# Kernel optimization log

Hardware: AMD Instinct MI355X
Metric: run time of the kernel (lower is better)

The kernel has to match this reference:

```python
import jax, jax.numpy as jnp
import numpy as np

NEG_SLOPE = 0.01  # torch LeakyReLU default
VAR = 0.1


def _leaky(z):
    return jnp.where(z >= 0, z, NEG_SLOPE * z)


def _sconv(theta, bias, L, x):
    # theta: (C_out, C_in, 2), L: (M, M), x: (B, C_in, M)
    Lx = jnp.einsum('mn,bin->bim', L, x)                     # degree-1 Laplacian term
    y = jnp.einsum('oi,bim->bom', theta[:, :, 0], x) \
        + jnp.einsum('oi,bim->bom', theta[:, :, 1], Lx)
    if bias is not None:
        y = y + bias
    return y


def setup_inputs() -> dict:
    key = jax.random.key(0)
    ks = iter(jax.random.split(key, 32))
    B, Cin = 8, 4
    Ms = [2000, 6000, 4000]
    inp = {}
    for d, M in enumerate(Ms):
        inp[f'L{d}'] = jax.random.normal(next(ks), (M, M), jnp.float32) / np.sqrt(M)
        inp[f'x{d}'] = jax.random.normal(next(ks), (B, Cin, M), jnp.float32)
        inp[f'th{d}_1'] = VAR * jax.random.normal(next(ks), (16, 4, 2), jnp.float32)
        inp[f'b{d}_1'] = jnp.zeros((1, 16, 1), jnp.float32)
        inp[f'th{d}_2'] = VAR * jax.random.normal(next(ks), (32, 16, 2), jnp.float32)
    dims = [(96, 64), (64, 32), (32, 16), (16, 2)]
    for i, (din, dout) in enumerate(dims, start=1):
        bound = 1.0 / np.sqrt(din)
        inp[f'W{i}'] = jax.random.uniform(next(ks), (dout, din), jnp.float32, -bound, bound)
        inp[f'bb{i}'] = jax.random.uniform(next(ks), (dout,), jnp.float32, -bound, bound)
    return inp


def reference(L0, L1, L2, x0, x1, x2,
              th0_1, b0_1, th0_2,
              th1_1, b1_1, th1_2,
              th2_1, b2_1, th2_2,
              W1, bb1, W2, bb2, W3, bb3, W4, bb4):
    out0_1 = _sconv(th0_1, b0_1, L0, x0)
    out1_1 = _sconv(th1_1, b1_1, L1, x1)
    out2_1 = _sconv(th2_1, b2_1, L2, x2)
    out0_2 = _sconv(th0_2, None, L0, _leaky(out0_1))   # (B, 32, M0)
    out1_2 = _sconv(th1_2, None, L1, _leaky(out1_1))
    out2_2 = _sconv(th2_2, None, L2, _leaky(out2_1))
    # mean-pool over simplices, concat along channel dim -> (B, 96)
    pooled = jnp.concatenate([out0_2.mean(axis=2), out1_2.mean(axis=2), out2_2.mean(axis=2)], axis=1)
    h = pooled @ W1.T + bb1      # dropouts are identity at inference
    h = h @ W2.T + bb2
    h = h @ W3.T + bb3
    logits = h @ W4.T + bb4      # (B, 2)
    return (logits, out0_2, out1_2, out2_2)
```

## Files before the change

### kernel.cpp

```cpp
#include <hip/hip_runtime.h>
#include <stdint.h>

typedef __attribute__((ext_vector_type(4))) float f32x4;
typedef __attribute__((ext_vector_type(8))) __bf16 bf16x8;

constexpr int MS_[3] = {2000, 6000, 4000};
constexpr int MP_[3] = {2048, 6144, 4096};
constexpr int RB_[3] = {32, 96, 64};
constexpr int NTILE = 192;
constexpr long long OUT_OFF_[3] = {16, 512016, 2048016};

constexpr int S1_[3] = {8, 16, 16};
constexpr int KS1_[3] = {256, 384, 256};
constexpr int NG1 = 1536 + 1024 + 256;
constexpr int KS2_[3] = {512, 1536, 1024};
constexpr int NG2 = 768 + 512 + 256;

__device__ __forceinline__ unsigned short f2bf(float f) {
  __bf16 b = (__bf16)f;
  return *reinterpret_cast<unsigned short*>(&b);
}

__device__ __forceinline__ void gload_lds16(const void* g, void* l) {
  __builtin_amdgcn_global_load_lds(
      (const __attribute__((address_space(1))) unsigned int*)g,
      (__attribute__((address_space(3))) unsigned int*)l, 16, 0, 0);
}

__device__ __forceinline__ void bar_pin() {
  __builtin_amdgcn_s_barrier();
  __builtin_amdgcn_sched_barrier(0);
}

__device__ __forceinline__ void tile_decode(int bid, int& d, int& t) {
  if (bid < RB_[0]) { d = 0; t = bid; }
  else if (bid < RB_[0] + RB_[1]) { d = 1; t = bid - RB_[0]; }
  else { d = 2; t = bid - RB_[0] - RB_[1]; }
}

struct PrepArgs {
  const float* x[3];
  unsigned short* xT[3];
  float* zero0; int zero_n;
};

__global__ __launch_bounds__(256) void prep_k(PrepArgs pa) {
  int d, t; tile_decode(blockIdx.x, d, t);
  const int M = MS_[d], Mp = MP_[d];
  const float* x = pa.x[d];
  unsigned short* xT = pa.xT[d];
  const int tid = threadIdx.x;
  const int m0 = t * 64;
  const int ml = tid & 63, cg = tid >> 6;
  const int m = m0 + ml;
  const bool valid = m < M;
#pragma unroll
  for (int it = 0; it < 8; ++it) {
    int c = it * 4 + cg;
    float v = valid ? x[(size_t)c * M + m] : 0.f;
    xT[(size_t)c * Mp + m] = f2bf(v);
  }
  if (blockIdx.x == 0) {
    for (int i = tid; i < pa.zero_n; i += 256) pa.zero0[i] = 0.f;
  }
}

struct GArgs {
  const float* L[3];
  const unsigned short* B[3];
  float* P[3];
};

template <int PASS>
__global__ __launch_bounds__(256, 2) void gemm_k(GArgs ga) {
  int bid = blockIdx.x;
  int d, r, s, nh = 0;
  if constexpr (PASS == 1) {
    if (bid < 1536) { d = 1; r = bid % 96; s = bid / 96; }
    else if (bid < 2560) { bid -= 1536; d = 2; r = bid % 64; s = bid / 64; }
    else { bid -= 2560; d = 0; r = bid % 32; s = bid / 32; }
  } else {
    if (bid < 768) { d = 1; r = bid % 96; int q = bid / 96; nh = q & 1; s = q >> 1; }
    else if (bid < 1280) { bid -= 768; d = 2; r = bid % 64; int q = bid / 64; nh = q & 1; s = q >> 1; }
    else { bid -= 1280; d = 0; r = bid % 32; int q = bid / 32; nh = q & 1; s = q >> 1; }
  }
  const int M = MS_[d], Mp = MP_[d];
  const int KS = (PASS == 1) ? KS1_[d] : KS2_[d];
  const int ns = KS >> 6;
  constexpr int BN = (PASS == 1) ? 32 : 64;
  constexpr int PW = (PASS == 1) ? 32 : 128;
  constexpr int RING = (PASS == 1) ? 4 : 3;
  constexpr int NR = BN / 16;
  constexpr int BI = BN / 32;

  const float* __restrict__ Lp = ga.L[d];
  const unsigned short* __restrict__ Bt = ga.B[d];
  float* __restrict__ Pp = ga.P[d];

  const int m0 = r * 64;
  const int kt0 = s * KS;

  __shared__ __align__(16) char Al[RING][64 * 256];
  __shared__ __align__(16) char Bl[RING][BN * 128];

  const int tid = threadIdx.x;
  const int lane = tid & 63;
  const int wave = tid >> 6;
  const int lr = lane & 15, lk = lane >> 4;

  const float* pAsrc[4];
  int koffA[4];
#pragma unroll
  for (int j = 0; j < 4; ++j) {
    int ldsb = j * 4096 + tid * 16;
    int row = ldsb >> 8;
    int inner = (ldsb & 255) ^ ((row & 7) << 5);
    int grow = m0 + row;
    if (grow > M - 1) grow = M - 1;
    pAsrc[j] = Lp + (size_t)grow * M;
    koffA[j] = inner >> 2;
  }
  const unsigned short* srcB[BI];
#pragma unroll
  for (int j = 0; j < BI; ++j) {
    int ldsb = j * 4096 + tid * 16;
    int col = ldsb >> 7;
    int inner = (ldsb & 127) ^ ((col & 7) << 4);
    srcB[j] = Bt + (size_t)(nh * 64 + col) * Mp + (inner >> 1);
  }

  f32x4 acc[NR];
#pragma unroll
  for (int n = 0; n < NR; ++n) acc[n] = (f32x4){0.f, 0.f, 0.f, 0.f};

  auto mstep = [&](int x) { return x < ns ? x : ns - 1; };
  auto stage = [&](int slot, int step) {
    const int kt = kt0 + step * 64;
#pragma unroll
    for (int j = 0; j < 4; ++j) {
      int gk = kt + koffA[j];
      if (gk + 4 > M) gk = 0;
      gload_lds16(pAsrc[j] + gk, &Al[slot][j * 4096 + tid * 16]);
    }
#pragma unroll
    for (int j = 0; j < BI; ++j)
      gload_lds16(srcB[j] + kt, &Bl[slot][j * 4096 + tid * 16]);
  };
  auto compute = [&](int slot) {
    const char* Ab = &Al[slot][0];
    const char* Bb = &Bl[slot][0];
    const int rowl = wave * 16 + lr;
    const int abase = rowl * 256;
    const int aswz = (rowl & 7) << 5;
    bf16x8 af[2];
#pragma unroll
    for (int kk = 0; kk < 2; ++kk) {
      int off = abase + ((kk * 128 + lk * 32) ^ aswz);
      f32x4 v0 = *reinterpret_cast<const f32x4*>(Ab + off);
      f32x4 v1 = *reinterpret_cast<const f32x4*>(Ab + off + 16);
#pragma unroll
      for (int j = 0; j < 4; ++j) {
        af[kk][j] = (__bf16)v0[j];
        af[kk][4 + j] = (__bf16)v1[j];
      }
    }
#pragma unroll
    for (int nr = 0; nr < NR; ++nr) {
      const int col = nr * 16 + lr;
      const int bbase = col * 128, bswz = (col & 7) << 4;
      bf16x8 b0 = *reinterpret_cast<const bf16x8*>(Bb + bbase + ((lk * 16) ^ bswz));
      bf16x8 b1 = *reinterpret_cast<const bf16x8*>(Bb + bbase + ((64 + lk * 16) ^ bswz));
      acc[nr] = __builtin_amdgcn_mfma_f32_16x16x32_bf16(af[0], b0, acc[nr], 0, 0, 0);
      acc[nr] = __builtin_amdgcn_mfma_f32_16x16x32_bf16(af[1], b1, acc[nr], 0, 0, 0);
    }
  };

  stage(0, 0);
  stage(1, mstep(1));
  if constexpr (RING == 4) stage(2, mstep(2));

  for (int t = 0; t < ns; ++t) {
    if constexpr (PASS == 1) asm volatile("s_waitcnt vmcnt(10)" ::: "memory");
    else                     asm volatile("s_waitcnt vmcnt(6)" ::: "memory");
    bar_pin();
    stage((t + RING - 1) % RING, mstep(t + RING - 1));
    compute(t % RING);
  }

  const int rowb = m0 + wave * 16 + lk * 4;
#pragma unroll
  for (int nr = 0; nr < NR; ++nr) {
    const int cc = (PASS == 1 ? 0 : nh * 64) + nr * 16 + lr;
#pragma unroll
    for (int j = 0; j < 4; ++j)
      Pp[((size_t)s * Mp + rowb + j) * PW + cc] = acc[nr][j];
  }
}

struct EpiAArgs {
  const float* part1[3];
  const float* x[3];
  const float* th1[3];
  const float* b1[3];
  unsigned short* zT[3];
};

__global__ __launch_bounds__(256) void epiA_k(EpiAArgs ea) {
  int d, t; tile_decode(blockIdx.x, d, t);
  const int M = MS_[d], Mp = MP_[d];
  const int m0 = t * 64;
  __shared__ float Ys[32 * 66];
  __shared__ float Xs[32 * 66];
  const int tid = threadIdx.x;
  const float* part = ea.part1[d];
  const size_t st = (size_t)Mp * 32;
  const int S1 = S1_[d];
#pragma unroll
  for (int it = 0; it < 8; ++it) {
    int idx = it * 256 + tid;
    int m = idx >> 5, c = idx & 31;
    size_t base = (size_t)(m0 + m) * 32 + c;
    float ssum = 0.f;
    for (int s5 = 0; s5 < S1; ++s5) ssum += part[s5 * st + base];
    Ys[c * 66 + m] = ssum;
  }
  {
    const float* x = ea.x[d];
    int m = tid & 63, cg = tid >> 6;
    bool valid = (m0 + m) < M;
#pragma unroll
    for (int it = 0; it < 8; ++it) {
      int c = it * 4 + cg;
      Xs[c * 66 + m] = valid ? x[(size_t)c * M + m0 + m] : 0.f;
    }
  }
  __syncthreads();
  const float* th = ea.th1[d];
  const float* bias = ea.b1[d];
  unsigned short* zT = ea.zT[d];
  const int m = tid & 63, cog = tid >> 6;
  const bool valid = (m0 + m) < M;
#pragma unroll
  for (int it = 0; it < 32; ++it) {
    int co = it * 4 + cog;
    int o = co & 15, b = co >> 4;
    float a = bias[o];
#pragma unroll
    for (int i = 0; i < 4; ++i) {
      int ci = b * 4 + i;
      a += th[(o * 4 + i) * 2] * Xs[ci * 66 + m] + th[(o * 4 + i) * 2 + 1] * Ys[ci * 66 + m];
    }
    float zz = (a >= 0.f) ? a : 0.01f * a;
    zT[(size_t)co * Mp + m0 + m] = valid ? f2bf(zz) : (unsigned short)0;
  }
}

struct EpiBArgs {
  const float* part2[3];
  const unsigned short* zT[3];
  const float* th2[3];
  float* out;
  float* csz;
  float* csy;
};

__global__ __launch_bounds__(256) void epiB_k(EpiBArgs eb) {
  int d, t; tile_decode(blockIdx.x, d, t);
  const int M = MS_[d], Mp = MP_[d];
  const int m0 = t * 64;
  __shared__ float Ys[128 * 66];
  __shared__ float red[256];
  const int tid = threadIdx.x;
  const float* part = eb.part2[d];
  float csum = 0.f;
#pragma unroll
  for (int it = 0; it < 32; ++it) {
    int idx = it * 256 + tid;
    int m = idx >> 7, c = idx & 127;
    size_t base = (size_t)(m0 + m) * 128 + c;
    size_t st = (size_t)Mp * 128;
    float ssum = part[base] + part[st + base] + part[2 * st + base] + part[3 * st + base];
    Ys[c * 66 + m] = ssum;
    if (m0 + m < M) csum += ssum;
  }
  red[tid] = csum;
  __syncthreads();
  if (tid < 128) atomicAdd(&eb.csy[d * 128 + tid], red[tid] + red[tid + 128]);

  const unsigned short* zT = eb.zT[d];
  const float* th = eb.th2[d];
  float* outp = eb.out + OUT_OFF_[d];
  const int m = tid & 63, g = tid >> 6;
  const bool valid = (m0 + m) < M;
#pragma unroll
  for (int bb = 0; bb < 2; ++bb) {
    int b = g * 2 + bb;
    float zv[16], yv[16];
#pragma unroll
    for (int o1 = 0; o1 < 16; ++o1) {
      int c = b * 16 + o1;
      unsigned short raw = zT[(size_t)c * Mp + m0 + m];
      __bf16 bf = *reinterpret_cast<__bf16*>(&raw);
      zv[o1] = (float)bf;
      yv[o1] = Ys[c * 66 + m];
    }
#pragma unroll
    for (int o1 = 0; o1 < 16; ++o1) {
      float v = zv[o1];
#pragma unroll
      for (int off = 32; off > 0; off >>= 1) v += __shfl_xor(v, off, 64);
      if (m == 0) atomicAdd(&eb.csz[d * 128 + b * 16 + o1], v);
    }
#pragma unroll
    for (int o2 = 0; o2 < 32; ++o2) {
      float v = 0.f;
#pragma unroll
      for (int o1 = 0; o1 < 16; ++o1)
        v += th[(o2 * 16 + o1) * 2] * zv[o1] + th[(o2 * 16 + o1) * 2 + 1] * yv[o1];
      if (valid) outp[(size_t)(b * 32 + o2) * M + m0 + m] = v;
    }
  }
}

struct MlpArgs {
  const float* csz; const float* csy;
  const float* th2[3];
  const float* W1; const float* b1;
  const float* W2; const float* b2;
  const float* W3; const float* b3;
  const float* W4; const float* b4;
  float* out;
};

__global__ __launch_bounds__(256) void mlp_k(MlpArgs ma) {
  __shared__ float pl[8][96];
  __shared__ float h1[8][64];
  __shared__ float h2[8][32];
  __shared__ float h3[8][16];
  const int tid = threadIdx.x;
  for (int id = tid; id < 768; id += 256) {
    int d = id >> 8, rem = id & 255, b = rem >> 5, o2 = rem & 31;
    const float* th = ma.th2[d];
    float invM = 1.f / (float)MS_[d];
    float v = 0.f;
    for (int o1 = 0; o1 < 16; ++o1)
      v += th[(o2 * 16 + o1) * 2] * ma.csz[d * 128 + b * 16 + o1] +
           th[(o2 * 16 + o1) * 2 + 1] * ma.csy[d * 128 + b * 16 + o1];
    pl[b][d * 32 + o2] = v * invM;
  }
  __syncthreads();
  for (int id = tid; id < 512; id += 256) {
    int b = id >> 6, j = id & 63;
    float v = ma.b1[j];
    for (int k = 0; k < 96; ++k) v += pl[b][k] * ma.W1[j * 96 + k];
    h1[b][j] = v;
  }
  __syncthreads();
  {
    int b = tid >> 5, j = tid & 31;
    float v = ma.b2[j];
    for (int k = 0; k < 64; ++k) v += h1[b][k] * ma.W2[j * 64 + k];
    h2[b][j] = v;
  }
  __syncthreads();
  if (tid < 128) {
    int b = tid >> 4, j = tid & 15;
    float v = ma.b3[j];
    for (int k = 0; k < 32; ++k) v += h2[b][k] * ma.W3[j * 32 + k];
    h3[b][j] = v;
  }
  __syncthreads();
  if (tid < 16) {
    int b = tid >> 1, j = tid & 1;
    float v = ma.b4[j];
    for (int k = 0; k < 16; ++k) v += h3[b][k] * ma.W4[j * 16 + k];
    ma.out[tid] = v;
  }
}

extern "C" void kernel_launch(void* const* d_in, const int* in_sizes, int n_in,
                              void* d_out, int out_size, void* d_ws, size_t ws_size,
                              hipStream_t stream) {
  (void)in_sizes; (void)n_in; (void)out_size; (void)ws_size;
  const float* L[3]   = {(const float*)d_in[0], (const float*)d_in[5], (const float*)d_in[10]};
  const float* x[3]   = {(const float*)d_in[1], (const float*)d_in[6], (const float*)d_in[11]};
  const float* th1[3] = {(const float*)d_in[2], (const float*)d_in[7], (const float*)d_in[12]};
  const float* b1[3]  = {(const float*)d_in[3], (const float*)d_in[8], (const float*)d_in[13]};
  const float* th2[3] = {(const float*)d_in[4], (const float*)d_in[9], (const float*)d_in[14]};
  const float* W1 = (const float*)d_in[15]; const float* bb1 = (const float*)d_in[16];
  const float* W2 = (const float*)d_in[17]; const float* bb2 = (const float*)d_in[18];
  const float* W3 = (const float*)d_in[19]; const float* bb3 = (const float*)d_in[20];
  const float* W4 = (const float*)d_in[21]; const float* bb4 = (const float*)d_in[22];
  float* out = (float*)d_out;

  char* ws = (char*)d_ws;
  size_t off = 0;
  auto alloc = [&](size_t bytes) {
    size_t r = off;
    off = (off + bytes + 255) & ~(size_t)255;
    return r;
  };
  const int MPs[3] = {2048, 6144, 4096};
  unsigned short* xT[3]; unsigned short* zT[3]; float* pb[3];
  for (int d = 0; d < 3; ++d) xT[d] = (unsigned short*)(ws + alloc((size_t)32 * MPs[d] * 2));
  for (int d = 0; d < 3; ++d) zT[d] = (unsigned short*)(ws + alloc((size_t)128 * MPs[d] * 2));
  for (int d = 0; d < 3; ++d) pb[d] = (float*)(ws + alloc((size_t)16 * MPs[d] * 32 * 4));
  float* csz = (float*)(ws + alloc((size_t)3 * 128 * 4));
  float* csy = (float*)(ws + alloc((size_t)3 * 128 * 4));

  PrepArgs pa;
  for (int d = 0; d < 3; ++d) { pa.x[d] = x[d]; pa.xT[d] = xT[d]; }
  pa.zero0 = csz; pa.zero_n = 768;
  prep_k<<<NTILE, 256, 0, stream>>>(pa);

  GArgs g1;
  for (int d = 0; d < 3; ++d) { g1.L[d] = L[d]; g1.B[d] = xT[d]; g1.P[d] = pb[d]; }
  gemm_k<1><<<NG1, 256, 0, stream>>>(g1);

  EpiAArgs ea;
  for (int d = 0; d < 3; ++d) {
    ea.part1[d] = pb[d]; ea.x[d] = x[d]; ea.th1[d] = th1[d]; ea.b1[d] = b1[d]; ea.zT[d] = zT[d];
  }
  epiA_k<<<NTILE, 256, 0, stream>>>(ea);

  GArgs g2;
  for (int d = 0; d < 3; ++d) { g2.L[d] = L[d]; g2.B[d] = zT[d]; g2.P[d] = pb[d]; }
  gemm_k<2><<<NG2, 256, 0, stream>>>(g2);

  EpiBArgs eb;
  for (int d = 0; d < 3; ++d) { eb.part2[d] = pb[d]; eb.zT[d] = zT[d]; eb.th2[d] = th2[d]; }
  eb.out = out; eb.csz = csz; eb.csy = csy;
  epiB_k<<<NTILE, 256, 0, stream>>>(eb);

  MlpArgs ma;
  ma.csz = csz; ma.csy = csy;
  for (int d = 0; d < 3; ++d) ma.th2[d] = th2[d];
  ma.W1 = W1; ma.b1 = bb1; ma.W2 = W2; ma.b2 = bb2;
  ma.W3 = W3; ma.b3 = bb3; ma.W4 = W4; ma.b4 = bb4;
  ma.out = out;
  mlp_k<<<1, 256, 0, stream>>>(ma);
}
```

Measured before the change: 226.1 us.

## Pre-convert Laplacians to bf16 once and widen pass-2 GEMM tile to 128 columns

Adds a conversion kernel that writes each fp32 Laplacian to a bf16 copy in workspace. Both GEMM passes then stream the bf16 copy, halving A-operand traffic and dropping the per-step fp32-to-bf16 conversion in the inner loop. Pass 2 now covers all 128 columns in one block instead of splitting into two 64-column halves, so L is read once per pass rather than twice. The cost is an extra full read of L in fp32 plus a bf16 write before pass 1; ring depths, wait counts and occupancy are retuned, and the old path is kept as a fallback when the workspace is too small.

```diff
diff --git a/kernel.cpp b/kernel.cpp
--- a/kernel.cpp
+++ b/kernel.cpp
@@ -14,7 +14,8 @@
 constexpr int KS1_[3] = {256, 384, 256};
 constexpr int NG1 = 1536 + 1024 + 256;
 constexpr int KS2_[3] = {512, 1536, 1024};
-constexpr int NG2 = 768 + 512 + 256;
+constexpr int NG2 = 384 + 256 + 128;
+constexpr int NCONV = 2304 + 1024 + 256;
 
 __device__ __forceinline__ unsigned short f2bf(float f) {
   __bf16 b = (__bf16)f;
@@ -32,10 +33,42 @@
   __builtin_amdgcn_sched_barrier(0);
 }
 
+template <int W>
+__device__ __forceinline__ void wait_w() {
+  if constexpr (W == 0) asm volatile("s_waitcnt vmcnt(0)" ::: "memory");
+  else if constexpr (W == 5) asm volatile("s_waitcnt vmcnt(5)" ::: "memory");
+  else if constexpr (W == 6) asm volatile("s_waitcnt vmcnt(6)" ::: "memory");
+}
+
 __device__ __forceinline__ void tile_decode(int bid, int& d, int& t) {
   if (bid < RB_[0]) { d = 0; t = bid; }
   else if (bid < RB_[0] + RB_[1]) { d = 1; t = bid - RB_[0]; }
   else { d = 2; t = bid - RB_[0] - RB_[1]; }
+}
+
+struct ConvArgs {
+  const float* src[3];
+  unsigned short* dst[3];
+};
+
+__global__ __launch_bounds__(256) void conv_k(ConvArgs ca) {
+  int bid = blockIdx.x;
+  int d, lb, nb;
+  if (bid < 2304) { d = 1; lb = bid; nb = 2304; }
+  else if (bid < 3328) { d = 2; lb = bid - 2304; nb = 1024; }
+  else { d = 0; lb = bid - 3328; nb = 256; }
+  const float* __restrict__ s = ca.src[d];
+  unsigned short* __restrict__ o = ca.dst[d];
+  const long long n8 = (long long)MS_[d] * MS_[d] / 8;
+  for (long long i = (long long)lb * 256 + threadIdx.x; i < n8; i += (long long)nb * 256) {
+    const float* p = s + i * 8;
+    f32x4 v0 = *reinterpret_cast<const f32x4*>(p);
+    f32x4 v1 = *reinterpret_cast<const f32x4*>(p + 4);
+    union { unsigned short u[8]; int4 q; } pk;
+#pragma unroll
+    for (int j = 0; j < 4; ++j) { pk.u[j] = f2bf(v0[j]); pk.u[4 + j] = f2bf(v1[j]); }
+    *reinterpret_cast<int4*>(o + i * 8) = pk.q;
+  }
 }
 
 struct PrepArgs {
@@ -67,40 +100,43 @@
 
 struct GArgs {
   const float* L[3];
+  const unsigned short* Lb[3];
   const unsigned short* B[3];
   float* P[3];
 };
 
-template <int PASS>
-__global__ __launch_bounds__(256, 2) void gemm_k(GArgs ga) {
+template <int PASS, bool ABF>
+__global__ __launch_bounds__(256, (PASS == 1 && ABF) ? 3 : 2) void gemm_k(GArgs ga) {
   int bid = blockIdx.x;
-  int d, r, s, nh = 0;
+  int d, r, s;
   if constexpr (PASS == 1) {
     if (bid < 1536) { d = 1; r = bid % 96; s = bid / 96; }
     else if (bid < 2560) { bid -= 1536; d = 2; r = bid % 64; s = bid / 64; }
     else { bid -= 2560; d = 0; r = bid % 32; s = bid / 32; }
   } else {
-    if (bid < 768) { d = 1; r = bid % 96; int q = bid / 96; nh = q & 1; s = q >> 1; }
-    else if (bid < 1280) { bid -= 768; d = 2; r = bid % 64; int q = bid / 64; nh = q & 1; s = q >> 1; }
-    else { bid -= 1280; d = 0; r = bid % 32; int q = bid / 32; nh = q & 1; s = q >> 1; }
+    if (bid < 384) { d = 1; r = bid % 96; s = bid / 96; }
+    else if (bid < 640) { bid -= 384; d = 2; r = bid % 64; s = bid / 64; }
+    else { bid -= 640; d = 0; r = bid % 32; s = bid / 32; }
   }
   const int M = MS_[d], Mp = MP_[d];
   const int KS = (PASS == 1) ? KS1_[d] : KS2_[d];
   const int ns = KS >> 6;
-  constexpr int BN = (PASS == 1) ? 32 : 64;
-  constexpr int PW = (PASS == 1) ? 32 : 128;
-  constexpr int RING = (PASS == 1) ? 4 : 3;
+  constexpr int BN = (PASS == 1) ? 32 : 128;
+  constexpr int PW = BN;
   constexpr int NR = BN / 16;
-  constexpr int BI = BN / 32;
-
-  const float* __restrict__ Lp = ga.L[d];
+  constexpr int BIB = BN / 32;
+  constexpr int BIA = ABF ? 2 : 4;
+  constexpr int RING = (PASS == 1) ? (ABF ? 4 : 3) : (ABF ? 3 : 2);
+  constexpr int ABYT = ABF ? 8192 : 16384;
+  constexpr int W = (PASS == 1) ? (ABF ? 6 : 5) : (ABF ? 6 : 0);
+
   const unsigned short* __restrict__ Bt = ga.B[d];
   float* __restrict__ Pp = ga.P[d];
 
   const int m0 = r * 64;
   const int kt0 = s * KS;
 
-  __shared__ __align__(16) char Al[RING][64 * 256];
+  __shared__ __align__(16) char Al[RING][ABYT];
   __shared__ __align__(16) char Bl[RING][BN * 128];
 
   const int tid = threadIdx.x;
@@ -108,25 +144,34 @@
   const int wave = tid >> 6;
   const int lr = lane & 15, lk = lane >> 4;
 
-  const float* pAsrc[4];
-  int koffA[4];
-#pragma unroll
-  for (int j = 0; j < 4; ++j) {
+  const char* rowA[BIA];
+  int koffA[BIA];
+#pragma unroll
+  for (int j = 0; j < BIA; ++j) {
     int ldsb = j * 4096 + tid * 16;
-    int row = ldsb >> 8;
-    int inner = (ldsb & 255) ^ ((row & 7) << 5);
+    int row, koff;
+    if constexpr (ABF) {
+      row = ldsb >> 7;
+      int inner = (ldsb & 127) ^ ((row & 7) << 4);
+      koff = inner >> 1;
+    } else {
+      row = ldsb >> 8;
+      int inner = (ldsb & 255) ^ ((row & 7) << 5);
+      koff = inner >> 2;
+    }
     int grow = m0 + row;
     if (grow > M - 1) grow = M - 1;
-    pAsrc[j] = Lp + (size_t)grow * M;
-    koffA[j] = inner >> 2;
-  }
-  const unsigned short* srcB[BI];
-#pragma unroll
-  for (int j = 0; j < BI; ++j) {
+    if constexpr (ABF) rowA[j] = (const char*)(ga.Lb[d] + (size_t)grow * M);
+    else               rowA[j] = (const char*)(ga.L[d] + (size_t)grow * M);
+    koffA[j] = koff;
+  }
+  const unsigned short* srcB[BIB];
+#pragma unroll
+  for (int j = 0; j < BIB; ++j) {
     int ldsb = j * 4096 + tid * 16;
     int col = ldsb >> 7;
     int inner = (ldsb & 127) ^ ((col & 7) << 4);
-    srcB[j] = Bt + (size_t)(nh * 64 + col) * Mp + (inner >> 1);
+    srcB[j] = Bt + (size_t)col * Mp + (inner >> 1);
   }
 
   f32x4 acc[NR];
@@ -137,31 +182,37 @@
   auto stage = [&](int slot, int step) {
     const int kt = kt0 + step * 64;
 #pragma unroll
-    for (int j = 0; j < 4; ++j) {
+    for (int j = 0; j < BIA; ++j) {
       int gk = kt + koffA[j];
-      if (gk + 4 > M) gk = 0;
-      gload_lds16(pAsrc[j] + gk, &Al[slot][j * 4096 + tid * 16]);
-    }
-#pragma unroll
-    for (int j = 0; j < BI; ++j)
+      if constexpr (ABF) { if (gk + 8 > M) gk = 0; }
+      else               { if (gk + 4 > M) gk = 0; }
+      gload_lds16(rowA[j] + (size_t)gk * (ABF ? 2 : 4), &Al[slot][j * 4096 + tid * 16]);
+    }
+#pragma unroll
+    for (int j = 0; j < BIB; ++j)
       gload_lds16(srcB[j] + kt, &Bl[slot][j * 4096 + tid * 16]);
   };
   auto compute = [&](int slot) {
     const char* Ab = &Al[slot][0];
     const char* Bb = &Bl[slot][0];
     const int rowl = wave * 16 + lr;
-    const int abase = rowl * 256;
-    const int aswz = (rowl & 7) << 5;
     bf16x8 af[2];
-#pragma unroll
-    for (int kk = 0; kk < 2; ++kk) {
-      int off = abase + ((kk * 128 + lk * 32) ^ aswz);
-      f32x4 v0 = *reinterpret_cast<const f32x4*>(Ab + off);
-      f32x4 v1 = *reinterpret_cast<const f32x4*>(Ab + off + 16);
-#pragma unroll
-      for (int j = 0; j < 4; ++j) {
-        af[kk][j] = (__bf16)v0[j];
-        af[kk][4 + j] = (__bf16)v1[j];
+    if constexpr (ABF) {
+      const int base = rowl * 128, swz = (rowl & 7) << 4;
+      af[0] = *reinterpret_cast<const bf16x8*>(Ab + base + ((lk * 16) ^ swz));
+      af[1] = *reinterpret_cast<const bf16x8*>(Ab + base + ((64 + lk * 16) ^ swz));
+    } else {
+      const int base = rowl * 256, swz = (rowl & 7) << 5;
+#pragma unroll
+      for (int kk = 0; kk < 2; ++kk) {
+        int off = base + ((kk * 128 + lk * 32) ^ swz);
+        f32x4 v0 = *reinterpret_cast<const f32x4*>(Ab + off);
+        f32x4 v1 = *reinterpret_cast<const f32x4*>(Ab + off + 16);
+#pragma unroll
+        for (int j = 0; j < 4; ++j) {
+          af[kk][j] = (__bf16)v0[j];
+          af[kk][4 + j] = (__bf16)v1[j];
+        }
       }
     }
 #pragma unroll
@@ -176,12 +227,11 @@
   };
 
   stage(0, 0);
-  stage(1, mstep(1));
-  if constexpr (RING == 4) stage(2, mstep(2));
+  if constexpr (RING >= 3) stage(1, mstep(1));
+  if constexpr (RING >= 4) stage(2, mstep(2));
 
   for (int t = 0; t < ns; ++t) {
-    if constexpr (PASS == 1) asm volatile("s_waitcnt vmcnt(10)" ::: "memory");
-    else                     asm volatile("s_waitcnt vmcnt(6)" ::: "memory");
+    wait_w<W>();
     bar_pin();
     stage((t + RING - 1) % RING, mstep(t + RING - 1));
     compute(t % RING);
@@ -190,7 +240,7 @@
   const int rowb = m0 + wave * 16 + lk * 4;
 #pragma unroll
   for (int nr = 0; nr < NR; ++nr) {
-    const int cc = (PASS == 1 ? 0 : nh * 64) + nr * 16 + lr;
+    const int cc = nr * 16 + lr;
 #pragma unroll
     for (int j = 0; j < 4; ++j)
       Pp[((size_t)s * Mp + rowb + j) * PW + cc] = acc[nr][j];
@@ -381,7 +431,7 @@
 extern "C" void kernel_launch(void* const* d_in, const int* in_sizes, int n_in,
                               void* d_out, int out_size, void* d_ws, size_t ws_size,
                               hipStream_t stream) {
-  (void)in_sizes; (void)n_in; (void)out_size; (void)ws_size;
+  (void)in_sizes; (void)n_in; (void)out_size;
   const float* L[3]   = {(const float*)d_in[0], (const float*)d_in[5], (const float*)d_in[10]};
   const float* x[3]   = {(const float*)d_in[1], (const float*)d_in[6], (const float*)d_in[11]};
   const float* th1[3] = {(const float*)d_in[2], (const float*)d_in[7], (const float*)d_in[12]};
@@ -407,15 +457,30 @@
   for (int d = 0; d < 3; ++d) pb[d] = (float*)(ws + alloc((size_t)16 * MPs[d] * 32 * 4));
   float* csz = (float*)(ws + alloc((size_t)3 * 128 * 4));
   float* csy = (float*)(ws + alloc((size_t)3 * 128 * 4));
+  unsigned short* Lb[3];
+  for (int d = 0; d < 3; ++d)
+    Lb[d] = (unsigned short*)(ws + alloc((size_t)MS_[d] * MS_[d] * 2));
+  const bool use_bf = (off <= ws_size);
 
   PrepArgs pa;
   for (int d = 0; d < 3; ++d) { pa.x[d] = x[d]; pa.xT[d] = xT[d]; }
   pa.zero0 = csz; pa.zero_n = 768;
   prep_k<<<NTILE, 256, 0, stream>>>(pa);
 
-  GArgs g1;
-  for (int d = 0; d < 3; ++d) { g1.L[d] = L[d]; g1.B[d] = xT[d]; g1.P[d] = pb[d]; }
-  gemm_k<1><<<NG1, 256, 0, stream>>>(g1);
+  GArgs ga;
+  for (int d = 0; d < 3; ++d) {
+    ga.L[d] = L[d]; ga.Lb[d] = Lb[d]; ga.P[d] = pb[d];
+  }
+
+  if (use_bf) {
+    ConvArgs ca;
+    for (int d = 0; d < 3; ++d) { ca.src[d] = L[d]; ca.dst[d] = Lb[d]; }
+    conv_k<<<NCONV, 256, 0, stream>>>(ca);
+  }
+
+  for (int d = 0; d < 3; ++d) ga.B[d] = xT[d];
+  if (use_bf) gemm_k<1, true><<<NG1, 256, 0, stream>>>(ga);
+  else        gemm_k<1, false><<<NG1, 256, 0, stream>>>(ga);
 
   EpiAArgs ea;
   for (int d = 0; d < 3; ++d) {
@@ -423,9 +488,9 @@
   }
   epiA_k<<<NTILE, 256, 0, stream>>>(ea);
 
-  GArgs g2;
-  for (int d = 0; d < 3; ++d) { g2.L[d] = L[d]; g2.B[d] = zT[d]; g2.P[d] = pb[d]; }
-  gemm_k<2><<<NG2, 256, 0, stream>>>(g2);
+  for (int d = 0; d < 3; ++d) ga.B[d] = zT[d];
+  if (use_bf) gemm_k<2, true><<<NG2, 256, 0, stream>>>(ga);
+  else        gemm_k<2, false><<<NG2, 256, 0, stream>>>(ga);
 
   EpiBArgs eb;
   for (int d = 0; d < 3; ++d) { eb.part2[d] = pb[d]; eb.zT[d] = zT[d]; eb.th2[d] = th2[d]; }
```

Result: slower. 257.3 us (+13.8%).

## Reduce split-K factor, use 2x2 wave tiling in pass 2, swizzle blocks across XCDs

Applied to the files above, without the earlier changes.

Pass 1 split-K drops from 8/16 to 4 slices and pass 2 from 4 to 2, so fewer partial sums are written and reduced. Pass 2 now assigns each wave a 32x32 sub-tile, reusing A and B fragments across two MFMA rows and columns. Block indices are remapped so consecutive blocks spread across the 8 XCDs. The cost is fewer workgroups (768 per pass) and longer K loops per block, which may cut parallelism and latency hiding.

```diff
diff --git a/kernel.cpp b/kernel.cpp
--- a/kernel.cpp
+++ b/kernel.cpp
@@ -10,11 +10,10 @@
 constexpr int NTILE = 192;
 constexpr long long OUT_OFF_[3] = {16, 512016, 2048016};
 
-constexpr int S1_[3] = {8, 16, 16};
-constexpr int KS1_[3] = {256, 384, 256};
-constexpr int NG1 = 1536 + 1024 + 256;
-constexpr int KS2_[3] = {512, 1536, 1024};
-constexpr int NG2 = 768 + 512 + 256;
+constexpr int KS1_[3] = {512, 1536, 1024};
+constexpr int NG1 = 384 + 256 + 128;
+constexpr int KS2_[3] = {1024, 3072, 2048};
+constexpr int NG2 = 384 + 256 + 128;
 
 __device__ __forceinline__ unsigned short f2bf(float f) {
   __bf16 b = (__bf16)f;
@@ -30,6 +29,18 @@
 __device__ __forceinline__ void bar_pin() {
   __builtin_amdgcn_s_barrier();
   __builtin_amdgcn_sched_barrier(0);
+}
+
+template <int W>
+__device__ __forceinline__ void wait_w() {
+  if constexpr (W == 6)  asm volatile("s_waitcnt vmcnt(6)" ::: "memory");
+  else if constexpr (W == 10) asm volatile("s_waitcnt vmcnt(10)" ::: "memory");
+  else asm volatile("s_waitcnt vmcnt(0)" ::: "memory");
+}
+
+__device__ __forceinline__ int xcd_swz(int bid, int nwg) {
+  int cpx = nwg >> 3;
+  return (bid & 7) * cpx + (bid >> 3);
 }
 
 __device__ __forceinline__ void tile_decode(int bid, int& d, int& t) {
@@ -73,25 +84,25 @@
 
 template <int PASS>
 __global__ __launch_bounds__(256, 2) void gemm_k(GArgs ga) {
-  int bid = blockIdx.x;
+  int bid = xcd_swz(blockIdx.x, (PASS == 1) ? NG1 : NG2);
   int d, r, s, nh = 0;
   if constexpr (PASS == 1) {
-    if (bid < 1536) { d = 1; r = bid % 96; s = bid / 96; }
-    else if (bid < 2560) { bid -= 1536; d = 2; r = bid % 64; s = bid / 64; }
-    else { bid -= 2560; d = 0; r = bid % 32; s = bid / 32; }
+    if (bid < 384) { d = 1; r = bid % 96; s = bid / 96; }
+    else if (bid < 640) { bid -= 384; d = 2; r = bid % 64; s = bid / 64; }
+    else { bid -= 640; d = 0; r = bid % 32; s = bid / 32; }
   } else {
-    if (bid < 768) { d = 1; r = bid % 96; int q = bid / 96; nh = q & 1; s = q >> 1; }
-    else if (bid < 1280) { bid -= 768; d = 2; r = bid % 64; int q = bid / 64; nh = q & 1; s = q >> 1; }
-    else { bid -= 1280; d = 0; r = bid % 32; int q = bid / 32; nh = q & 1; s = q >> 1; }
+    if (bid < 384) { d = 1; r = bid % 96; int q = bid / 96; nh = q & 1; s = q >> 1; }
+    else if (bid < 640) { bid -= 384; d = 2; r = bid % 64; int q = bid / 64; nh = q & 1; s = q >> 1; }
+    else { bid -= 640; d = 0; r = bid % 32; int q = bid / 32; nh = q & 1; s = q >> 1; }
   }
   const int M = MS_[d], Mp = MP_[d];
   const int KS = (PASS == 1) ? KS1_[d] : KS2_[d];
   const int ns = KS >> 6;
   constexpr int BN = (PASS == 1) ? 32 : 64;
   constexpr int PW = (PASS == 1) ? 32 : 128;
+  constexpr int BIB = BN / 32;
   constexpr int RING = (PASS == 1) ? 4 : 3;
-  constexpr int NR = BN / 16;
-  constexpr int BI = BN / 32;
+  constexpr int W = (PASS == 1) ? 10 : 6;
 
   const float* __restrict__ Lp = ga.L[d];
   const unsigned short* __restrict__ Bt = ga.B[d];
@@ -100,15 +111,16 @@
   const int m0 = r * 64;
   const int kt0 = s * KS;
 
-  __shared__ __align__(16) char Al[RING][64 * 256];
+  __shared__ __align__(16) char Al[RING][16384];
   __shared__ __align__(16) char Bl[RING][BN * 128];
 
   const int tid = threadIdx.x;
   const int lane = tid & 63;
   const int wave = tid >> 6;
   const int lr = lane & 15, lk = lane >> 4;
-
-  const float* pAsrc[4];
+  const int wr = wave >> 1, wc = wave & 1;
+
+  const float* rowA[4];
   int koffA[4];
 #pragma unroll
   for (int j = 0; j < 4; ++j) {
@@ -117,21 +129,22 @@
     int inner = (ldsb & 255) ^ ((row & 7) << 5);
     int grow = m0 + row;
     if (grow > M - 1) grow = M - 1;
-    pAsrc[j] = Lp + (size_t)grow * M;
+    rowA[j] = Lp + (size_t)grow * M;
     koffA[j] = inner >> 2;
   }
-  const unsigned short* srcB[BI];
-#pragma unroll
-  for (int j = 0; j < BI; ++j) {
+  const unsigned short* srcB[BIB];
+#pragma unroll
+  for (int j = 0; j < BIB; ++j) {
     int ldsb = j * 4096 + tid * 16;
     int col = ldsb >> 7;
     int inner = (ldsb & 127) ^ ((col & 7) << 4);
     srcB[j] = Bt + (size_t)(nh * 64 + col) * Mp + (inner >> 1);
   }
 
-  f32x4 acc[NR];
-#pragma unroll
-  for (int n = 0; n < NR; ++n) acc[n] = (f32x4){0.f, 0.f, 0.f, 0.f};
+  constexpr int NACC = (PASS == 1) ? 2 : 4;
+  f32x4 acc[NACC];
+#pragma unroll
+  for (int n = 0; n < NACC; ++n) acc[n] = (f32x4){0.f, 0.f, 0.f, 0.f};
 
   auto mstep = [&](int x) { return x < ns ? x : ns - 1; };
   auto stage = [&](int slot, int step) {
@@ -140,60 +153,94 @@
     for (int j = 0; j < 4; ++j) {
       int gk = kt + koffA[j];
       if (gk + 4 > M) gk = 0;
-      gload_lds16(pAsrc[j] + gk, &Al[slot][j * 4096 + tid * 16]);
-    }
-#pragma unroll
-    for (int j = 0; j < BI; ++j)
+      gload_lds16(rowA[j] + gk, &Al[slot][j * 4096 + tid * 16]);
+    }
+#pragma unroll
+    for (int j = 0; j < BIB; ++j)
       gload_lds16(srcB[j] + kt, &Bl[slot][j * 4096 + tid * 16]);
   };
+
+  auto readAf = [&](const char* Ab, int rowl, int kk) -> bf16x8 {
+    const int base = rowl * 256, swz = (rowl & 7) << 5;
+    int off = base + ((kk * 128 + lk * 32) ^ swz);
+    f32x4 v0 = *reinterpret_cast<const f32x4*>(Ab + off);
+    f32x4 v1 = *reinterpret_cast<const f32x4*>(Ab + off + 16);
+    bf16x8 af;
+#pragma unroll
+    for (int j = 0; j < 4; ++j) { af[j] = (__bf16)v0[j]; af[4 + j] = (__bf16)v1[j]; }
+    return af;
+  };
+  auto readB = [&](const char* Bb, int col, int half) -> bf16x8 {
+    const int bbase = col * 128, bswz = (col & 7) << 4;
+    return *reinterpret_cast<const bf16x8*>(Bb + bbase + ((half * 64 + lk * 16) ^ bswz));
+  };
+
   auto compute = [&](int slot) {
     const char* Ab = &Al[slot][0];
     const char* Bb = &Bl[slot][0];
-    const int rowl = wave * 16 + lr;
-    const int abase = rowl * 256;
-    const int aswz = (rowl & 7) << 5;
-    bf16x8 af[2];
-#pragma unroll
-    for (int kk = 0; kk < 2; ++kk) {
-      int off = abase + ((kk * 128 + lk * 32) ^ aswz);
-      f32x4 v0 = *reinterpret_cast<const f32x4*>(Ab + off);
-      f32x4 v1 = *reinterpret_cast<const f32x4*>(Ab + off + 16);
-#pragma unroll
-      for (int j = 0; j < 4; ++j) {
-        af[kk][j] = (__bf16)v0[j];
-        af[kk][4 + j] = (__bf16)v1[j];
+    if constexpr (PASS == 1) {
+      const int rowl = wave * 16 + lr;
+      bf16x8 a0 = readAf(Ab, rowl, 0), a1 = readAf(Ab, rowl, 1);
+#pragma unroll
+      for (int nr = 0; nr < 2; ++nr) {
+        bf16x8 b0 = readB(Bb, nr * 16 + lr, 0);
+        bf16x8 b1 = readB(Bb, nr * 16 + lr, 1);
+        acc[nr] = __builtin_amdgcn_mfma_f32_16x16x32_bf16(a0, b0, acc[nr], 0, 0, 0);
+        acc[nr] = __builtin_amdgcn_mfma_f32_16x16x32_bf16(a1, b1, acc[nr], 0, 0, 0);
       }
-    }
-#pragma unroll
-    for (int nr = 0; nr < NR; ++nr) {
-      const int col = nr * 16 + lr;
-      const int bbase = col * 128, bswz = (col & 7) << 4;
-      bf16x8 b0 = *reinterpret_cast<const bf16x8*>(Bb + bbase + ((lk * 16) ^ bswz));
-      bf16x8 b1 = *reinterpret_cast<const bf16x8*>(Bb + bbase + ((64 + lk * 16) ^ bswz));
-      acc[nr] = __builtin_amdgcn_mfma_f32_16x16x32_bf16(af[0], b0, acc[nr], 0, 0, 0);
-      acc[nr] = __builtin_amdgcn_mfma_f32_16x16x32_bf16(af[1], b1, acc[nr], 0, 0, 0);
+    } else {
+      bf16x8 af[2][2];
+#pragma unroll
+      for (int mr = 0; mr < 2; ++mr) {
+        af[mr][0] = readAf(Ab, wr * 32 + mr * 16 + lr, 0);
+        af[mr][1] = readAf(Ab, wr * 32 + mr * 16 + lr, 1);
+      }
+#pragma unroll
+      for (int nr = 0; nr < 2; ++nr) {
+        const int col = wc * 32 + nr * 16 + lr;
+        bf16x8 b0 = readB(Bb, col, 0);
+        bf16x8 b1 = readB(Bb, col, 1);
+#pragma unroll
+        for (int mr = 0; mr < 2; ++mr) {
+          acc[mr * 2 + nr] = __builtin_amdgcn_mfma_f32_16x16x32_bf16(af[mr][0], b0, acc[mr * 2 + nr], 0, 0, 0);
+          acc[mr * 2 + nr] = __builtin_amdgcn_mfma_f32_16x16x32_bf16(af[mr][1], b1, acc[mr * 2 + nr], 0, 0, 0);
+        }
+      }
     }
   };
 
   stage(0, 0);
   stage(1, mstep(1));
-  if constexpr (RING == 4) stage(2, mstep(2));
+  if constexpr (RING >= 4) stage(2, mstep(2));
 
   for (int t = 0; t < ns; ++t) {
-    if constexpr (PASS == 1) asm volatile("s_waitcnt vmcnt(10)" ::: "memory");
-    else                     asm volatile("s_waitcnt vmcnt(6)" ::: "memory");
+    wait_w<W>();
     bar_pin();
     stage((t + RING - 1) % RING, mstep(t + RING - 1));
     compute(t % RING);
   }
 
-  const int rowb = m0 + wave * 16 + lk * 4;
-#pragma unroll
-  for (int nr = 0; nr < NR; ++nr) {
-    const int cc = (PASS == 1 ? 0 : nh * 64) + nr * 16 + lr;
-#pragma unroll
-    for (int j = 0; j < 4; ++j)
-      Pp[((size_t)s * Mp + rowb + j) * PW + cc] = acc[nr][j];
+  if constexpr (PASS == 1) {
+    const int rowb = m0 + wave * 16 + lk * 4;
+#pragma unroll
+    for (int nr = 0; nr < 2; ++nr) {
+      const int cc = nr * 16 + lr;
+#pragma unroll
+      for (int j = 0; j < 4; ++j)
+        Pp[((size_t)s * Mp + rowb + j) * PW + cc] = acc[nr][j];
+    }
+  } else {
+#pragma unroll
+    for (int mr = 0; mr < 2; ++mr) {
+      const int rowb = m0 + wr * 32 + mr * 16 + lk * 4;
+#pragma unroll
+      for (int nr = 0; nr < 2; ++nr) {
+        const int cc = nh * 64 + wc * 32 + nr * 16 + lr;
+#pragma unroll
+        for (int j = 0; j < 4; ++j)
+          Pp[((size_t)s * Mp + rowb + j) * PW + cc] = acc[mr * 2 + nr][j];
+      }
+    }
   }
 }
 
@@ -214,14 +261,12 @@
   const int tid = threadIdx.x;
   const float* part = ea.part1[d];
   const size_t st = (size_t)Mp * 32;
-  const int S1 = S1_[d];
 #pragma unroll
   for (int it = 0; it < 8; ++it) {
     int idx = it * 256 + tid;
     int m = idx >> 5, c = idx & 31;
     size_t base = (size_t)(m0 + m) * 32 + c;
-    float ssum = 0.f;
-    for (int s5 = 0; s5 < S1; ++s5) ssum += part[s5 * st + base];
+    float ssum = part[base] + part[st + base] + part[2 * st + base] + part[3 * st + base];
     Ys[c * 66 + m] = ssum;
   }
   {
@@ -279,7 +324,7 @@
     int m = idx >> 7, c = idx & 127;
     size_t base = (size_t)(m0 + m) * 128 + c;
     size_t st = (size_t)Mp * 128;
-    float ssum = part[base] + part[st + base] + part[2 * st + base] + part[3 * st + base];
+    float ssum = part[base] + part[st + base];
     Ys[c * 66 + m] = ssum;
     if (m0 + m < M) csum += ssum;
   }
@@ -404,7 +449,7 @@
   unsigned short* xT[3]; unsigned short* zT[3]; float* pb[3];
   for (int d = 0; d < 3; ++d) xT[d] = (unsigned short*)(ws + alloc((size_t)32 * MPs[d] * 2));
   for (int d = 0; d < 3; ++d) zT[d] = (unsigned short*)(ws + alloc((size_t)128 * MPs[d] * 2));
-  for (int d = 0; d < 3; ++d) pb[d] = (float*)(ws + alloc((size_t)16 * MPs[d] * 32 * 4));
+  for (int d = 0; d < 3; ++d) pb[d] = (float*)(ws + alloc((size_t)MPs[d] * 1024));
   float* csz = (float*)(ws + alloc((size_t)3 * 128 * 4));
   float* csy = (float*)(ws + alloc((size_t)3 * 128 * 4));
 
@@ -413,9 +458,11 @@
   pa.zero0 = csz; pa.zero_n = 768;
   prep_k<<<NTILE, 256, 0, stream>>>(pa);
 
-  GArgs g1;
-  for (int d = 0; d < 3; ++d) { g1.L[d] = L[d]; g1.B[d] = xT[d]; g1.P[d] = pb[d]; }
-  gemm_k<1><<<NG1, 256, 0, stream>>>(g1);
+  GArgs ga;
+  for (int d = 0; d < 3; ++d) { ga.L[d] = L[d]; ga.P[d] = pb[d]; }
+
+  for (int d = 0; d < 3; ++d) ga.B[d] = xT[d];
+  gemm_k<1><<<NG1, 256, 0, stream>>>(ga);
 
   EpiAArgs ea;
   for (int d = 0; d < 3; ++d) {
@@ -423,9 +470,8 @@
   }
   epiA_k<<<NTILE, 256, 0, stream>>>(ea);
 
-  GArgs g2;
-  for (int d = 0; d < 3; ++d) { g2.L[d] = L[d]; g2.B[d] = zT[d]; g2.P[d] = pb[d]; }
-  gemm_k<2><<<NG2, 256, 0, stream>>>(g2);
+  for (int d = 0; d < 3; ++d) ga.B[d] = zT[d];
+  gemm_k<2><<<NG2, 256, 0, stream>>>(ga);
 
   EpiBArgs eb;
   for (int d = 0; d < 3; ++d) { eb.part2[d] = pb[d]; eb.zT[d] = zT[d]; eb.th2[d] = th2[d]; }
```

New measurement: 233.8 us. 3.4% more time.
